# Optimization experiments

Measured on AMD Instinct MI355X. Metric: run time of the kernel, lower is better.

Reference implementation:

```python
import jax, jax.numpy as jnp
import numpy as np

B, T, C = 2, 2048, 2048
H = 16
D = C // H  # 128 head dim
EPS = 1.1920929e-07  # torch RMSNorm default eps for fp32 (finfo.eps)
ROPE_BASE = 1000000.0


def setup_inputs() -> dict:
    key = jax.random.key(0)
    k1, k2, k3 = jax.random.split(key, 3)
    x = jax.random.normal(k1, (B, T, C), dtype=jnp.float32)
    w_qkv = jax.random.normal(k2, (C, 3 * C), dtype=jnp.float32) * (C ** -0.5)
    w_proj = jax.random.normal(k3, (C, C), dtype=jnp.float32) * (C ** -0.5)
    q_norm_w = jnp.ones((D,), dtype=jnp.float32)
    k_norm_w = jnp.ones((D,), dtype=jnp.float32)
    return {"x": x, "w_qkv": w_qkv, "w_proj": w_proj,
            "q_norm_w": q_norm_w, "k_norm_w": k_norm_w}


def _rms_norm(x, w):
    var = jnp.mean(jnp.square(x), axis=-1, keepdims=True)
    return x * jax.lax.rsqrt(var + EPS) * w


def _rope_tables(t_len, d_head, dtype):
    inv_freq = 1.0 / (ROPE_BASE ** (jnp.arange(0, d_head, 2, dtype=jnp.float32) / d_head))
    t = jnp.arange(t_len, dtype=jnp.float32)
    freqs = jnp.einsum('i,j->ij', t, inv_freq)          # [T, D/2]
    emb = jnp.concatenate([freqs, freqs], axis=-1)      # [T, D]
    return jnp.cos(emb).astype(dtype), jnp.sin(emb).astype(dtype)


def _rotate_half(x):
    x1, x2 = x[..., : x.shape[-1] // 2], x[..., x.shape[-1] // 2:]
    return jnp.concatenate([-x2, x1], axis=-1)


def reference(x, w_qkv, w_proj, q_norm_w, k_norm_w):
    b, t, c = x.shape
    qkv = x @ w_qkv                                     # [B, T, 3C]
    q, k, v = jnp.split(qkv, 3, axis=-1)
    # [B, H, T, D]
    q = q.reshape(b, t, H, D).transpose(0, 2, 1, 3)
    k = k.reshape(b, t, H, D).transpose(0, 2, 1, 3)
    v = v.reshape(b, t, H, D).transpose(0, 2, 1, 3)
    q = _rms_norm(q, q_norm_w)
    k = _rms_norm(k, k_norm_w)
    cos, sin = _rope_tables(t, D, x.dtype)              # [T, D]
    q = q * cos + _rotate_half(q) * sin
    k = k * cos + _rotate_half(k) * sin
    # NOTE: module uses scale = 1/d_head, not 1/sqrt(d_head)
    scale = 1.0 / D
    att = jnp.einsum('bhqd,bhkd->bhqk', q, k) * scale   # [B, H, T, T]
    causal = jnp.tril(jnp.ones((t, t), dtype=bool))
    att = jnp.where(causal, att, jnp.finfo(att.dtype).min)
    att = jax.nn.softmax(att, axis=-1)
    y = jnp.einsum('bhqk,bhkd->bhqd', att, v)           # [B, H, T, D]
    y = y.transpose(0, 2, 1, 3).reshape(b, t, c)
    return y @ w_proj
```

## Files before the change

### kernel.cpp

```cpp
#include <hip/hip_runtime.h>
#include <stdint.h>

#define Bb   2
#define Tt   2048
#define Cc_  2048
#define Hh   16
#define Dd   128
#define Mm_  4096
#define N1   6144
#define EPSf 1.1920929e-07f
#define SCALE (1.0f/128.0f)

typedef __bf16 bf16;
typedef __attribute__((ext_vector_type(8))) __bf16 bf16x8;
typedef __attribute__((ext_vector_type(4))) float  f32x4;

__device__ __forceinline__ void gl_lds16(const bf16* g, bf16* l) {
  __builtin_amdgcn_global_load_lds(
      (const __attribute__((address_space(1))) unsigned int*)g,
      (__attribute__((address_space(3))) unsigned int*)l, 16, 0, 0);
}

__global__ __launch_bounds__(256) void cvt_bf16(const float* __restrict__ in,
                                                bf16* __restrict__ out, int n) {
  int i = (blockIdx.x * 256 + threadIdx.x) * 4;
  if (i >= n) return;
  float4 v = *(const float4*)(in + i);
  union { bf16 h[4]; uint2 u; } o;
  o.h[0] = (bf16)v.x; o.h[1] = (bf16)v.y; o.h[2] = (bf16)v.z; o.h[3] = (bf16)v.w;
  *(uint2*)(out + i) = o.u;
}

__global__ __launch_bounds__(256) void transpose_cvt(const float* __restrict__ in,
                                                     bf16* __restrict__ out,
                                                     int R, int Cc) {
  __shared__ float tile[64][65];
  int c0 = blockIdx.x * 64, r0 = blockIdx.y * 64;
  int tid = threadIdx.x;
#pragma unroll
  for (int j = 0; j < 16; ++j) {
    int idx = tid + j * 256;
    int r = idx >> 6, c = idx & 63;
    tile[r][c] = in[(size_t)(r0 + r) * Cc + c0 + c];
  }
  __syncthreads();
#pragma unroll
  for (int j = 0; j < 16; ++j) {
    int idx = tid + j * 256;
    int rr = idx & 63, cc = idx >> 6;
    out[(size_t)(c0 + cc) * R + r0 + rr] = (bf16)tile[rr][cc];
  }
}

__global__ __launch_bounds__(256) void vtrans(const bf16* __restrict__ V,
                                              bf16* __restrict__ Vt_) {
  __shared__ bf16 tile[64][72];
  int bh = blockIdx.z, t0 = blockIdx.x * 64, d0 = blockIdx.y * 64;
  int tid = threadIdx.x;
#pragma unroll
  for (int j = 0; j < 2; ++j) {
    int idx = (j * 256 + tid) * 8;
    int r = idx >> 6, c = idx & 63;
    bf16x8 v = *(const bf16x8*)(V + ((size_t)bh * Tt + t0 + r) * Dd + d0 + c);
#pragma unroll
    for (int e = 0; e < 8; ++e) tile[r][c + e] = v[e];
  }
  __syncthreads();
#pragma unroll
  for (int j = 0; j < 2; ++j) {
    int idx = (j * 256 + tid) * 8;
    int dd = idx >> 6, tt = idx & 63;
    bf16x8 v;
#pragma unroll
    for (int e = 0; e < 8; ++e) v[e] = tile[tt + e][dd];
    *(bf16x8*)(Vt_ + ((size_t)bh * Dd + d0 + dd) * Tt + t0 + tt) = v;
  }
}

template <typename OutT>
__global__ __launch_bounds__(256) void gemm_bf16(const bf16* __restrict__ A,
                                                 const bf16* __restrict__ Bt,
                                                 OutT* __restrict__ Cm,
                                                 int Nn, int Kk) {
  __shared__ __align__(16) bf16 As[128 * 64];
  __shared__ __align__(16) bf16 Bs[128 * 64];
  const int tid = threadIdx.x;
  const int wave = tid >> 6, lane = tid & 63;
  const int quad = lane >> 4, li = lane & 15;
  const int wm = wave >> 1, wn = wave & 1;
  const int m0 = blockIdx.y * 128, n0 = blockIdx.x * 128;

  f32x4 acc[4][4] = {};

  for (int kt = 0; kt < Kk; kt += 64) {
    __syncthreads();
#pragma unroll
    for (int j = 0; j < 4; ++j) {
      int c = j * 256 + tid;
      int r = c >> 3, cc = c & 7;
      int gc = ((cc ^ (r & 7)) << 3);
      gl_lds16(A + (size_t)(m0 + r) * Kk + kt + gc, &As[c * 8]);
      gl_lds16(Bt + (size_t)(n0 + r) * Kk + kt + gc, &Bs[c * 8]);
    }
    __syncthreads();
#pragma unroll
    for (int kc = 0; kc < 2; ++kc) {
      bf16x8 af[4], bfr[4];
#pragma unroll
      for (int t = 0; t < 4; ++t) {
        int rowa = wm * 64 + t * 16 + li;
        af[t] = *(const bf16x8*)&As[rowa * 64 + (((kc * 4 + quad) ^ (rowa & 7)) << 3)];
        int rowb = wn * 64 + t * 16 + li;
        bfr[t] = *(const bf16x8*)&Bs[rowb * 64 + (((kc * 4 + quad) ^ (rowb & 7)) << 3)];
      }
#pragma unroll
      for (int mi = 0; mi < 4; ++mi)
#pragma unroll
        for (int ni = 0; ni < 4; ++ni)
          acc[mi][ni] = __builtin_amdgcn_mfma_f32_16x16x32_bf16(af[mi], bfr[ni],
                                                                acc[mi][ni], 0, 0, 0);
    }
  }
#pragma unroll
  for (int mi = 0; mi < 4; ++mi) {
    int row = m0 + wm * 64 + mi * 16 + quad * 4;
#pragma unroll
    for (int ni = 0; ni < 4; ++ni) {
      int col = n0 + wn * 64 + ni * 16 + li;
#pragma unroll
      for (int r = 0; r < 4; ++r)
        Cm[(size_t)(row + r) * Nn + col] = (OutT)acc[mi][ni][r];
    }
  }
}

__global__ __launch_bounds__(512, 2) void gemm256(const bf16* __restrict__ A,
                                                  const bf16* __restrict__ Bt,
                                                  bf16* __restrict__ Cm,
                                                  int Nn, int Kk) {
  __shared__ __align__(16) bf16 As[2][256 * 64];
  __shared__ __align__(16) bf16 Bs[2][256 * 64];
  const int tid = threadIdx.x;
  const int wave = tid >> 6, lane = tid & 63;
  const int quad = lane >> 4, li = lane & 15;
  const int wm = wave >> 2, wn = wave & 3;

  const int nwg = gridDim.x * gridDim.y;
  const int wg  = blockIdx.y * gridDim.x + blockIdx.x;
  const int swz = (wg & 7) * (nwg >> 3) + (wg >> 3);
  const int m0 = (swz / gridDim.x) * 256;
  const int n0 = (swz % gridDim.x) * 256;

  const int NT = Kk >> 6;
  const int lrow = lane >> 3;
  const int lchk = (lane & 7) ^ lrow;

  auto stageA = [&](int tt, int h, int cb) {
    int kt = (tt < NT ? tt : NT - 1) << 6;
#pragma unroll
    for (int j = 0; j < 2; ++j) {
      int seg = j * 8 + wave;
      int r0 = ((seg >> 3) << 7) + (h << 6) + ((seg & 7) << 3);
      gl_lds16(A + (size_t)(m0 + r0 + lrow) * Kk + kt + (lchk << 3),
               &As[cb][r0 * 64]);
    }
  };
  auto stageB = [&](int tt, int h, int cb) {
    int kt = (tt < NT ? tt : NT - 1) << 6;
#pragma unroll
    for (int j = 0; j < 2; ++j) {
      int seg = j * 8 + wave;
      int r0 = ((seg >> 2) << 6) + (h << 5) + ((seg & 3) << 3);
      gl_lds16(Bt + (size_t)(n0 + r0 + lrow) * Kk + kt + (lchk << 3),
               &Bs[cb][r0 * 64]);
    }
  };

  f32x4 acc[8][4] = {};
  bf16x8 afr[4][2], b0r[2][2], b1r[2][2];

  auto rdA = [&](int h, int cb) {
#pragma unroll
    for (int mi = 0; mi < 4; ++mi) {
      int r = wm * 128 + h * 64 + mi * 16 + li;
#pragma unroll
      for (int kc = 0; kc < 2; ++kc)
        afr[mi][kc] = *(const bf16x8*)&As[cb][r * 64 + (((kc * 4 + quad) ^ (r & 7)) << 3)];
    }
  };
  auto rdB = [&](int h, int cb, bf16x8 (&dst)[2][2]) {
#pragma unroll
    for (int nj = 0; nj < 2; ++nj) {
      int r = wn * 64 + h * 32 + nj * 16 + li;
#pragma unroll
      for (int kc = 0; kc < 2; ++kc)
        dst[nj][kc] = *(const bf16x8*)&Bs[cb][r * 64 + (((kc * 4 + quad) ^ (r & 7)) << 3)];
    }
  };
  auto mmac = [&](int mo, int no, bf16x8 (&b)[2][2]) {
    __builtin_amdgcn_s_setprio(1);
#pragma unroll
    for (int kc = 0; kc < 2; ++kc)
#pragma unroll
      for (int mi = 0; mi < 4; ++mi)
#pragma unroll
        for (int nj = 0; nj < 2; ++nj)
          acc[mo + mi][no + nj] = __builtin_amdgcn_mfma_f32_16x16x32_bf16(
              afr[mi][kc], b[nj][kc], acc[mo + mi][no + nj], 0, 0, 0);
    __builtin_amdgcn_s_setprio(0);
  };

  auto tile = [&](int t, int cur, int nxt) {
    rdA(0, cur); rdB(0, cur, b0r);
    stageA(t + 1, 1, nxt);
    asm volatile("s_waitcnt lgkmcnt(8)" ::: "memory");
    __builtin_amdgcn_s_barrier();
    asm volatile("s_waitcnt lgkmcnt(0)" ::: "memory");
    __builtin_amdgcn_sched_barrier(0);
    mmac(0, 0, b0r);
    __builtin_amdgcn_s_barrier();
    rdB(1, cur, b1r);
    stageA(t + 2, 0, cur);
    __builtin_amdgcn_s_barrier();
    asm volatile("s_waitcnt lgkmcnt(0)" ::: "memory");
    __builtin_amdgcn_sched_barrier(0);
    mmac(0, 2, b1r);
    __builtin_amdgcn_s_barrier();
    rdA(1, cur);
    stageB(t + 2, 0, cur);
    __builtin_amdgcn_s_barrier();
    asm volatile("s_waitcnt lgkmcnt(0)" ::: "memory");
    __builtin_amdgcn_sched_barrier(0);
    mmac(4, 2, b1r);
    __builtin_amdgcn_s_barrier();
    stageB(t + 2, 1, cur);
    __builtin_amdgcn_s_barrier();
    __builtin_amdgcn_sched_barrier(0);
    mmac(4, 0, b0r);
    asm volatile("s_waitcnt vmcnt(6)" ::: "memory");
    __builtin_amdgcn_s_barrier();
  };

  stageA(0, 0, 0); stageB(0, 0, 0); stageB(0, 1, 0); stageA(0, 1, 0);
  stageA(1, 0, 1); stageB(1, 0, 1); stageB(1, 1, 1);
  asm volatile("s_waitcnt vmcnt(6)" ::: "memory");
  __builtin_amdgcn_s_barrier();

  for (int t = 0; t < NT; t += 2) {
    tile(t, 0, 1);
    tile(t + 1, 1, 0);
  }
  asm volatile("s_waitcnt vmcnt(0)" ::: "memory");

#pragma unroll
  for (int mi = 0; mi < 8; ++mi) {
    int row = m0 + wm * 128 + mi * 16 + quad * 4;
#pragma unroll
    for (int nj = 0; nj < 4; ++nj) {
      int col = n0 + wn * 64 + nj * 16 + li;
#pragma unroll
      for (int r = 0; r < 4; ++r)
        Cm[(size_t)(row + r) * Nn + col] = (bf16)acc[mi][nj][r];
    }
  }
}

__global__ __launch_bounds__(256) void norm_rope_rearrange(
    const bf16* __restrict__ qkv, const float* __restrict__ qw,
    const float* __restrict__ kw, bf16* __restrict__ Qg,
    bf16* __restrict__ Kg, bf16* __restrict__ Vg) {
  int unit = blockIdx.x * 4 + (threadIdx.x >> 6);
  int lane = threadIdx.x & 63;
  int h = unit & 15;
  int bt = unit >> 4;
  int t = bt & 2047, b = bt >> 11;
  const bf16* base = qkv + (size_t)bt * N1 + h * Dd;
  float q1 = (float)base[lane], q2 = (float)base[lane + 64];
  float k1 = (float)base[Cc_ + lane], k2 = (float)base[Cc_ + lane + 64];
  float v1 = (float)base[2 * Cc_ + lane], v2 = (float)base[2 * Cc_ + lane + 64];
  float sq = q1 * q1 + q2 * q2;
  float sk = k1 * k1 + k2 * k2;
#pragma unroll
  for (int o = 1; o < 64; o <<= 1) { sq += __shfl_xor(sq, o); sk += __shfl_xor(sk, o); }
  float rq = rsqrtf(sq * (1.0f / 128.0f) + EPSf);
  float rk = rsqrtf(sk * (1.0f / 128.0f) + EPSf);
  q1 *= rq * qw[lane]; q2 *= rq * qw[lane + 64];
  k1 *= rk * kw[lane]; k2 *= rk * kw[lane + 64];
  float invf = exp2f((float)lane * (-19.9315685693241740f / 64.0f));
  float ang = (float)t * invf;
  float sn, cs;
  sincosf(ang, &sn, &cs);
  float qo1 = q1 * cs - q2 * sn, qo2 = q2 * cs + q1 * sn;
  float ko1 = k1 * cs - k2 * sn, ko2 = k2 * cs + k1 * sn;
  size_t o1 = ((size_t)(b * Hh + h) * Tt + t) * Dd + lane;
  Qg[o1] = (bf16)qo1; Qg[o1 + 64] = (bf16)qo2;
  Kg[o1] = (bf16)ko1; Kg[o1 + 64] = (bf16)ko2;
  Vg[o1] = (bf16)v1;  Vg[o1 + 64] = (bf16)v2;
}

__global__ __launch_bounds__(256, 3) void attn(const bf16* __restrict__ Qg,
                                               const bf16* __restrict__ Kg,
                                               const bf16* __restrict__ VgT,
                                               bf16* __restrict__ Yg) {
  __shared__ __align__(16) bf16 Kl[64 * 128];
  __shared__ __align__(16) bf16 Vl[128 * 64];
  __shared__ __align__(16) bf16 Pl[4 * 16 * 72];
  const int bh = blockIdx.x;
  const int qt = (int)gridDim.y - 1 - (int)blockIdx.y;
  const int b = bh >> 4, h = bh & 15;
  const int tid = threadIdx.x, wave = tid >> 6, lane = tid & 63;
  const int quad = lane >> 4, li = lane & 15;
  const int q0 = qt * 64;

  const bf16* Qbase = Qg + ((size_t)bh * Tt + q0 + wave * 16 + li) * Dd;
  bf16x8 qf[4];
#pragma unroll
  for (int kc = 0; kc < 4; ++kc) qf[kc] = *(const bf16x8*)(Qbase + kc * 32 + quad * 8);

  f32x4 o[8] = {};
  float L[4] = {};
  bf16* Pw = &Pl[wave * 16 * 72];

  for (int kt = 0; kt <= qt; ++kt) {
    const int k0 = kt * 64;
    __syncthreads();
#pragma unroll
    for (int j = 0; j < 4; ++j) {
      int c = j * 256 + tid;
      int r = c >> 4, cc = c & 15;
      gl_lds16(Kg + ((size_t)bh * Tt + k0 + r) * Dd + ((cc ^ (r & 7)) << 3), &Kl[c * 8]);
    }
#pragma unroll
    for (int j = 0; j < 4; ++j) {
      int c = j * 256 + tid;
      int r = c >> 3, cc = c & 7;
      gl_lds16(VgT + ((size_t)bh * Dd + r) * Tt + k0 + ((cc ^ (r & 7)) << 3), &Vl[c * 8]);
    }
    __syncthreads();

    f32x4 s4[4] = {};
#pragma unroll
    for (int nt = 0; nt < 4; ++nt) {
      int key = nt * 16 + li;
#pragma unroll
      for (int kc = 0; kc < 4; ++kc) {
        bf16x8 kf = *(const bf16x8*)&Kl[key * 128 + (((kc * 4 + quad) ^ (key & 7)) << 3)];
        s4[nt] = __builtin_amdgcn_mfma_f32_16x16x32_bf16(qf[kc], kf, s4[nt], 0, 0, 0);
      }
    }
    const bool diag = (kt == qt);
#pragma unroll
    for (int nt = 0; nt < 4; ++nt)
#pragma unroll
      for (int r = 0; r < 4; ++r) {
        float e = __expf(s4[nt][r] * SCALE);
        if (diag && (nt * 16 + li > wave * 16 + quad * 4 + r)) e = 0.f;
        L[r] += e;
        Pw[(quad * 4 + r) * 72 + nt * 16 + li] = (bf16)e;
      }
#pragma unroll
    for (int kc = 0; kc < 2; ++kc) {
      bf16x8 pf = *(const bf16x8*)&Pw[li * 72 + kc * 32 + quad * 8];
#pragma unroll
      for (int u = 0; u < 8; ++u) {
        bf16x8 vf = *(const bf16x8*)&Vl[(u * 16 + li) * 64 + (((kc * 4 + quad) ^ (li & 7)) << 3)];
        o[u] = __builtin_amdgcn_mfma_f32_16x16x32_bf16(pf, vf, o[u], 0, 0, 0);
      }
    }
  }

  float inv[4];
#pragma unroll
  for (int r = 0; r < 4; ++r) {
    float s0 = L[r];
#pragma unroll
    for (int off = 1; off < 16; off <<= 1) s0 += __shfl_xor(s0, off);
    inv[r] = 1.0f / s0;
  }
  int trow = q0 + wave * 16 + quad * 4;
#pragma unroll
  for (int u = 0; u < 8; ++u) {
    int col = h * Dd + u * 16 + li;
#pragma unroll
    for (int r = 0; r < 4; ++r)
      Yg[(size_t)(b * Tt + trow + r) * Cc_ + col] = (bf16)(o[u][r] * inv[r]);
  }
}

extern "C" void kernel_launch(void* const* d_in, const int* in_sizes, int n_in,
                              void* d_out, int out_size, void* d_ws, size_t ws_size,
                              hipStream_t stream) {
  const float* x      = (const float*)d_in[0];
  const float* w_qkv  = (const float*)d_in[1];
  const float* w_proj = (const float*)d_in[2];
  const float* qnw    = (const float*)d_in[3];
  const float* knw    = (const float*)d_in[4];
  float* out = (float*)d_out;

  bf16* xb     = (bf16*)d_ws;
  bf16* wqkvT  = xb + (size_t)Mm_ * Cc_;
  bf16* wprojT = wqkvT + (size_t)N1 * Cc_;
  bf16* qkv    = wprojT + (size_t)Cc_ * Cc_;
  bf16* Qg     = qkv + (size_t)Mm_ * N1;
  bf16* Kg     = Qg + (size_t)Bb * Hh * Tt * Dd;
  bf16* Vg     = Kg + (size_t)Bb * Hh * Tt * Dd;
  bf16* VgT    = xb;
  bf16* Yg     = qkv;

  hipLaunchKernelGGL(cvt_bf16, dim3((Mm_ * Cc_ / 4) / 256), dim3(256), 0, stream,
                     x, xb, Mm_ * Cc_);
  hipLaunchKernelGGL(transpose_cvt, dim3(N1 / 64, Cc_ / 64), dim3(256), 0, stream,
                     w_qkv, wqkvT, Cc_, N1);
  hipLaunchKernelGGL(transpose_cvt, dim3(Cc_ / 64, Cc_ / 64), dim3(256), 0, stream,
                     w_proj, wprojT, Cc_, Cc_);
  hipLaunchKernelGGL(gemm256, dim3(N1 / 256, Mm_ / 256), dim3(512), 0, stream,
                     xb, wqkvT, qkv, N1, Cc_);
  hipLaunchKernelGGL(norm_rope_rearrange, dim3(Bb * Tt * Hh / 4), dim3(256), 0, stream,
                     qkv, qnw, knw, Qg, Kg, Vg);
  hipLaunchKernelGGL(vtrans, dim3(Tt / 64, Dd / 64, Bb * Hh), dim3(256), 0, stream,
                     Vg, VgT);
  hipLaunchKernelGGL(attn, dim3(Bb * Hh, Tt / 64), dim3(256), 0, stream,
                     Qg, Kg, VgT, Yg);
  hipLaunchKernelGGL(gemm_bf16<float>, dim3(Cc_ / 128, Mm_ / 128), dim3(256), 0, stream,
                     Yg, wprojT, out, Cc_, Cc_);
}
```

Measured before the change: 391.0 us.

## Narrow gemm256 to 256x128 tiles, reuse for proj GEMM, prefetch K/V in attention

```diff
diff --git a/kernel.cpp b/kernel.cpp
--- a/kernel.cpp
+++ b/kernel.cpp
@@ -134,12 +134,13 @@
   }
 }
 
+template <typename OutT>
 __global__ __launch_bounds__(512, 2) void gemm256(const bf16* __restrict__ A,
                                                   const bf16* __restrict__ Bt,
-                                                  bf16* __restrict__ Cm,
+                                                  OutT* __restrict__ Cm,
                                                   int Nn, int Kk) {
   __shared__ __align__(16) bf16 As[2][256 * 64];
-  __shared__ __align__(16) bf16 Bs[2][256 * 64];
+  __shared__ __align__(16) bf16 Bs[2][128 * 64];
   const int tid = threadIdx.x;
   const int wave = tid >> 6, lane = tid & 63;
   const int quad = lane >> 4, li = lane & 15;
@@ -149,7 +150,7 @@
   const int wg  = blockIdx.y * gridDim.x + blockIdx.x;
   const int swz = (wg & 7) * (nwg >> 3) + (wg >> 3);
   const int m0 = (swz / gridDim.x) * 256;
-  const int n0 = (swz % gridDim.x) * 256;
+  const int n0 = (swz % gridDim.x) * 128;
 
   const int NT = Kk >> 6;
   const int lrow = lane >> 3;
@@ -165,19 +166,19 @@
                &As[cb][r0 * 64]);
     }
   };
-  auto stageB = [&](int tt, int h, int cb) {
+  auto stageB = [&](int tt, int cb) {
     int kt = (tt < NT ? tt : NT - 1) << 6;
 #pragma unroll
     for (int j = 0; j < 2; ++j) {
       int seg = j * 8 + wave;
-      int r0 = ((seg >> 2) << 6) + (h << 5) + ((seg & 3) << 3);
+      int r0 = seg << 3;
       gl_lds16(Bt + (size_t)(n0 + r0 + lrow) * Kk + kt + (lchk << 3),
                &Bs[cb][r0 * 64]);
     }
   };
 
-  f32x4 acc[8][4] = {};
-  bf16x8 afr[4][2], b0r[2][2], b1r[2][2];
+  f32x4 acc[8][2] = {};
+  bf16x8 afr[4][2], bfr[2][2];
 
   auto rdA = [&](int h, int cb) {
 #pragma unroll
@@ -188,16 +189,16 @@
         afr[mi][kc] = *(const bf16x8*)&As[cb][r * 64 + (((kc * 4 + quad) ^ (r & 7)) << 3)];
     }
   };
-  auto rdB = [&](int h, int cb, bf16x8 (&dst)[2][2]) {
+  auto rdB = [&](int cb) {
 #pragma unroll
     for (int nj = 0; nj < 2; ++nj) {
-      int r = wn * 64 + h * 32 + nj * 16 + li;
+      int r = wn * 32 + nj * 16 + li;
 #pragma unroll
       for (int kc = 0; kc < 2; ++kc)
-        dst[nj][kc] = *(const bf16x8*)&Bs[cb][r * 64 + (((kc * 4 + quad) ^ (r & 7)) << 3)];
-    }
-  };
-  auto mmac = [&](int mo, int no, bf16x8 (&b)[2][2]) {
+        bfr[nj][kc] = *(const bf16x8*)&Bs[cb][r * 64 + (((kc * 4 + quad) ^ (r & 7)) << 3)];
+    }
+  };
+  auto mmac = [&](int mo) {
     __builtin_amdgcn_s_setprio(1);
 #pragma unroll
     for (int kc = 0; kc < 2; ++kc)
@@ -205,44 +206,34 @@
       for (int mi = 0; mi < 4; ++mi)
 #pragma unroll
         for (int nj = 0; nj < 2; ++nj)
-          acc[mo + mi][no + nj] = __builtin_amdgcn_mfma_f32_16x16x32_bf16(
-              afr[mi][kc], b[nj][kc], acc[mo + mi][no + nj], 0, 0, 0);
+          acc[mo + mi][nj] = __builtin_amdgcn_mfma_f32_16x16x32_bf16(
+              afr[mi][kc], bfr[nj][kc], acc[mo + mi][nj], 0, 0, 0);
     __builtin_amdgcn_s_setprio(0);
   };
 
   auto tile = [&](int t, int cur, int nxt) {
-    rdA(0, cur); rdB(0, cur, b0r);
+    rdA(0, cur); rdB(cur);
     stageA(t + 1, 1, nxt);
     asm volatile("s_waitcnt lgkmcnt(8)" ::: "memory");
     __builtin_amdgcn_s_barrier();
     asm volatile("s_waitcnt lgkmcnt(0)" ::: "memory");
     __builtin_amdgcn_sched_barrier(0);
-    mmac(0, 0, b0r);
-    __builtin_amdgcn_s_barrier();
-    rdB(1, cur, b1r);
+    mmac(0);
+    asm volatile("s_waitcnt vmcnt(6)" ::: "memory");
+    __builtin_amdgcn_s_barrier();
+    rdA(1, cur);
     stageA(t + 2, 0, cur);
+    stageB(t + 2, cur);
     __builtin_amdgcn_s_barrier();
     asm volatile("s_waitcnt lgkmcnt(0)" ::: "memory");
     __builtin_amdgcn_sched_barrier(0);
-    mmac(0, 2, b1r);
-    __builtin_amdgcn_s_barrier();
-    rdA(1, cur);
-    stageB(t + 2, 0, cur);
-    __builtin_amdgcn_s_barrier();
-    asm volatile("s_waitcnt lgkmcnt(0)" ::: "memory");
-    __builtin_amdgcn_sched_barrier(0);
-    mmac(4, 2, b1r);
-    __builtin_amdgcn_s_barrier();
-    stageB(t + 2, 1, cur);
-    __builtin_amdgcn_s_barrier();
-    __builtin_amdgcn_sched_barrier(0);
-    mmac(4, 0, b0r);
+    mmac(4);
     asm volatile("s_waitcnt vmcnt(6)" ::: "memory");
     __builtin_amdgcn_s_barrier();
   };
 
-  stageA(0, 0, 0); stageB(0, 0, 0); stageB(0, 1, 0); stageA(0, 1, 0);
-  stageA(1, 0, 1); stageB(1, 0, 1); stageB(1, 1, 1);
+  stageA(0, 0, 0); stageB(0, 0); stageA(0, 1, 0);
+  stageA(1, 0, 1); stageB(1, 1);
   asm volatile("s_waitcnt vmcnt(6)" ::: "memory");
   __builtin_amdgcn_s_barrier();
 
@@ -256,11 +247,11 @@
   for (int mi = 0; mi < 8; ++mi) {
     int row = m0 + wm * 128 + mi * 16 + quad * 4;
 #pragma unroll
-    for (int nj = 0; nj < 4; ++nj) {
-      int col = n0 + wn * 64 + nj * 16 + li;
+    for (int nj = 0; nj < 2; ++nj) {
+      int col = n0 + wn * 32 + nj * 16 + li;
 #pragma unroll
       for (int r = 0; r < 4; ++r)
-        Cm[(size_t)(row + r) * Nn + col] = (bf16)acc[mi][nj][r];
+        Cm[(size_t)(row + r) * Nn + col] = (OutT)acc[mi][nj][r];
     }
   }
 }
@@ -321,22 +312,38 @@
   float L[4] = {};
   bf16* Pw = &Pl[wave * 16 * 72];
 
-  for (int kt = 0; kt <= qt; ++kt) {
-    const int k0 = kt * 64;
-    __syncthreads();
+  bf16x8 kreg[4];
+  auto loadK = [&](int k0) {
 #pragma unroll
     for (int j = 0; j < 4; ++j) {
       int c = j * 256 + tid;
       int r = c >> 4, cc = c & 15;
-      gl_lds16(Kg + ((size_t)bh * Tt + k0 + r) * Dd + ((cc ^ (r & 7)) << 3), &Kl[c * 8]);
-    }
+      kreg[j] = *(const bf16x8*)(Kg + ((size_t)bh * Tt + k0 + r) * Dd + ((cc ^ (r & 7)) << 3));
+    }
+  };
+  auto stageV = [&](int k0) {
 #pragma unroll
     for (int j = 0; j < 4; ++j) {
       int c = j * 256 + tid;
       int r = c >> 3, cc = c & 7;
       gl_lds16(VgT + ((size_t)bh * Dd + r) * Tt + k0 + ((cc ^ (r & 7)) << 3), &Vl[c * 8]);
     }
-    __syncthreads();
+  };
+
+  loadK(0);
+  stageV(0);
+
+  for (int kt = 0; kt <= qt; ++kt) {
+    asm volatile("s_waitcnt vmcnt(4)" ::: "memory");
+#pragma unroll
+    for (int j = 0; j < 4; ++j) {
+      int c = j * 256 + tid;
+      *(bf16x8*)&Kl[c * 8] = kreg[j];
+    }
+    if (kt < qt) loadK(kt * 64 + 64);
+    asm volatile("s_waitcnt lgkmcnt(0)" ::: "memory");
+    __builtin_amdgcn_s_barrier();
+    __builtin_amdgcn_sched_barrier(0);
 
     f32x4 s4[4] = {};
 #pragma unroll
@@ -358,6 +365,11 @@
         L[r] += e;
         Pw[(quad * 4 + r) * 72 + nt * 16 + li] = (bf16)e;
       }
+    if (kt < qt) { asm volatile("s_waitcnt vmcnt(4)" ::: "memory"); }
+    else         { asm volatile("s_waitcnt vmcnt(0)" ::: "memory"); }
+    __builtin_amdgcn_s_barrier();
+    __builtin_amdgcn_sched_barrier(0);
+
 #pragma unroll
     for (int kc = 0; kc < 2; ++kc) {
       bf16x8 pf = *(const bf16x8*)&Pw[li * 72 + kc * 32 + quad * 8];
@@ -367,6 +379,10 @@
         o[u] = __builtin_amdgcn_mfma_f32_16x16x32_bf16(pf, vf, o[u], 0, 0, 0);
       }
     }
+    asm volatile("" ::: "memory");
+    __builtin_amdgcn_s_barrier();
+    __builtin_amdgcn_sched_barrier(0);
+    if (kt < qt) stageV(kt * 64 + 64);
   }
 
   float inv[4];
@@ -413,7 +429,7 @@
                      w_qkv, wqkvT, Cc_, N1);
   hipLaunchKernelGGL(transpose_cvt, dim3(Cc_ / 64, Cc_ / 64), dim3(256), 0, stream,
                      w_proj, wprojT, Cc_, Cc_);
-  hipLaunchKernelGGL(gemm256, dim3(N1 / 256, Mm_ / 256), dim3(512), 0, stream,
+  hipLaunchKernelGGL(gemm256<bf16>, dim3(N1 / 128, Mm_ / 256), dim3(512), 0, stream,
                      xb, wqkvT, qkv, N1, Cc_);
   hipLaunchKernelGGL(norm_rope_rearrange, dim3(Bb * Tt * Hh / 4), dim3(256), 0, stream,
                      qkv, qnw, knw, Qg, Kg, Vg);
@@ -421,6 +437,6 @@
                      Vg, VgT);
   hipLaunchKernelGGL(attn, dim3(Bb * Hh, Tt / 64), dim3(256), 0, stream,
                      Qg, Kg, VgT, Yg);
-  hipLaunchKernelGGL(gemm_bf16<float>, dim3(Cc_ / 128, Mm_ / 128), dim3(256), 0, stream,
+  hipLaunchKernelGGL(gemm256<float>, dim3(Cc_ / 128, Mm_ / 256), dim3(512), 0, stream,
                      Yg, wprojT, out, Cc_, Cc_);
 }
```

Measured after the change: 376.6 us. 3.7% less time.
